# Kernel optimization log

Hardware: AMD Instinct MI355X
Metric: run time of the kernel (lower is better)

The kernel has to match this reference:

```python
import jax, jax.numpy as jnp
import numpy as np

N, E = 50000, 800000
IN_DIM, OUT_DIM, HEADS, ORDER = 128, 32, 4, 2
HID = OUT_DIM * HEADS  # 128
NEG_SLOPE = 0.2
LN_EPS = 1e-5


def setup_inputs() -> dict:
    key = jax.random.key(0)
    ks = jax.random.split(key, 16)
    inp = {
        'features': jax.random.normal(ks[0], (N, IN_DIM), jnp.float32),
        'src': jax.random.randint(ks[1], (E,), 0, N, jnp.int32),
        'dst': jax.random.randint(ks[2], (E,), 0, N, jnp.int32),
    }
    in_dims = [IN_DIM, HID]
    for i in range(ORDER):
        d_in = in_dims[i]
        s = 1.0 / np.sqrt(d_in)
        inp[f'W{i}'] = jax.random.normal(ks[3 + 5 * i], (d_in, HID), jnp.float32) * s
        inp[f'al{i}'] = jax.random.normal(ks[4 + 5 * i], (HEADS, OUT_DIM), jnp.float32) * 0.1
        inp[f'ar{i}'] = jax.random.normal(ks[5 + 5 * i], (HEADS, OUT_DIM), jnp.float32) * 0.1
        inp[f'b{i}'] = jnp.zeros((HID,), jnp.float32)
        inp[f'g{i}'] = jnp.ones((HID,), jnp.float32)
        inp[f'be{i}'] = jnp.zeros((HID,), jnp.float32)
    return inp


def _gat_layer(x, src, dst, W, al, ar, b):
    # x: [N, d_in] -> h: [N, H, D]
    h = (x @ W).reshape(N, HEADS, OUT_DIM)
    el = jnp.sum(h * al, axis=-1)  # [N, H]
    er = jnp.sum(h * ar, axis=-1)  # [N, H]
    e = jax.nn.leaky_relu(el[src] + er[dst], NEG_SLOPE)  # [E, H]
    # segment softmax over incoming edges of each dst node
    m = jax.ops.segment_max(e, dst, num_segments=N)  # [N, H]
    ex = jnp.exp(e - m[dst])  # [E, H]
    denom = jax.ops.segment_sum(ex, dst, num_segments=N)  # [N, H]
    alpha = ex / jnp.maximum(denom[dst], 1e-9)  # [E, H]
    msg = h[src] * alpha[:, :, None]  # [E, H, D]
    out = jax.ops.segment_sum(msg, dst, num_segments=N)  # [N, H, D]
    return out.reshape(N, HID) + b


def _layernorm(x, g, be):
    mu = jnp.mean(x, axis=-1, keepdims=True)
    var = jnp.mean(jnp.square(x - mu), axis=-1, keepdims=True)
    return (x - mu) * jax.lax.rsqrt(var + LN_EPS) * g + be


def reference(features, src, dst, W0, al0, ar0, b0, g0, be0, W1, al1, ar1, b1, g1, be1):
    feats = features
    params = [(W0, al0, ar0, b0, g0, be0), (W1, al1, ar1, b1, g1, be1)]
    for (W, al, ar, b, g, be) in params:
        feats = _gat_layer(feats, src, dst, W, al, ar, b)
        feats = _layernorm(feats, g, be)
        feats = jax.nn.elu(feats)
    return feats
```

## Files before the change

### kernel.cpp

```cpp
#include <hip/hip_runtime.h>
#include <hip/hip_bf16.h>

#define N_NODES 50000
#define E_EDGES 800000
#define HID 128
#define HEADS 4
#define NEG_SLOPE 0.2f
#define LN_EPS 1e-5f
#define PARAM_FLOATS 17024
#define NBUCK 196
#define BCAP 6144
#define BIN_CH 2048

__device__ __forceinline__ float bf2f(__hip_bfloat16 b) { return __bfloat162float(b); }
__device__ __forceinline__ float u2f(unsigned short u) {
    return __uint_as_float(((unsigned int)u) << 16);
}
__device__ __forceinline__ float leaky(float v) { return v > 0.f ? v : v * NEG_SLOPE; }

__device__ __forceinline__ unsigned int f2ord(float f) {
    unsigned int u = __float_as_uint(f);
    return (u & 0x80000000u) ? ~u : (u | 0x80000000u);
}
__device__ __forceinline__ float ord2f(unsigned int u) {
    u = (u & 0x80000000u) ? (u & 0x7FFFFFFFu) : ~u;
    return __uint_as_float(u);
}

__global__ __launch_bounds__(256) void detect_kernel(const unsigned int* __restrict__ w0,
                                                     unsigned int* __restrict__ flag,
                                                     unsigned int* __restrict__ gmax0,
                                                     unsigned int* __restrict__ gmax1) {
    int t = threadIdx.x;
    if (t < 4) {
        gmax0[t] = f2ord(-INFINITY);
        gmax1[t] = f2ord(-INFINITY);
    }
    int cnt = 0;
    for (int i = t; i < 4096; i += 256) {
        unsigned int lo = (w0[i] & 0xFFFFu) << 16;
        float v = fabsf(__uint_as_float(lo));
        if (v >= 1e-6f && v <= 1.0f) cnt++;
    }
    __shared__ int sh[4];
#pragma unroll
    for (int off = 32; off >= 1; off >>= 1) cnt += __shfl_xor(cnt, off);
    if ((t & 63) == 0) sh[t >> 6] = cnt;
    __syncthreads();
    if (t == 0) *flag = ((sh[0] + sh[1] + sh[2] + sh[3]) > 2048) ? 1u : 0u;
}

__device__ __forceinline__ float load_any(const void* p, int i, unsigned int isbf16) {
    return isbf16 ? bf2f(((const __hip_bfloat16*)p)[i]) : ((const float*)p)[i];
}

__global__ __launch_bounds__(256) void cvt_params_kernel(const void* W, const void* al,
                                                         const void* ar, const void* b,
                                                         const void* g, const void* be,
                                                         const unsigned int* __restrict__ flag,
                                                         float* __restrict__ out) {
    int i = blockIdx.x * 256 + threadIdx.x;
    if (i >= PARAM_FLOATS) return;
    unsigned int isb = *flag;
    const void* src; int off;
    if (i < 16384)      { src = W;  off = i; }
    else if (i < 16512) { src = al; off = i - 16384; }
    else if (i < 16640) { src = ar; off = i - 16512; }
    else if (i < 16768) { src = b;  off = i - 16640; }
    else if (i < 16896) { src = g;  off = i - 16768; }
    else                { src = be; off = i - 16896; }
    out[i] = load_any(src, off, isb);
}

__global__ __launch_bounds__(256) void bin_kernel(const int* __restrict__ src,
                                                  const int* __restrict__ dst,
                                                  int* __restrict__ bcnt,
                                                  int2* __restrict__ ebuf) {
    __shared__ int lh[NBUCK];
    __shared__ int lbase[NBUCK];
    int t = threadIdx.x;
    for (int i = t; i < NBUCK; i += 256) lh[i] = 0;
    __syncthreads();
    int e0 = blockIdx.x * BIN_CH;
    int n = min(BIN_CH, E_EDGES - e0);
    int s8[8], d8[8], rk[8];
#pragma unroll
    for (int j = 0; j < 8; ++j) {
        int k = j * 256 + t;
        if (k < n) {
            s8[j] = src[e0 + k];
            d8[j] = dst[e0 + k];
            rk[j] = atomicAdd(&lh[d8[j] >> 8], 1);
        }
    }
    __syncthreads();
    for (int i = t; i < NBUCK; i += 256) lbase[i] = atomicAdd(&bcnt[i], lh[i]);
    __syncthreads();
#pragma unroll
    for (int j = 0; j < 8; ++j) {
        int k = j * 256 + t;
        if (k < n) {
            int b = d8[j] >> 8;
            int pos = lbase[b] + rk[j];
            if (pos < BCAP) ebuf[b * BCAP + pos] = make_int2(s8[j], d8[j]);
        }
    }
}

__global__ __launch_bounds__(256) void bscan_kernel(const int* __restrict__ bcnt,
                                                    int* __restrict__ bbase) {
    int t = threadIdx.x;
    int lane = t & 63, wid = t >> 6;
    int v = (t < NBUCK) ? min(bcnt[t], BCAP) : 0;
    int x = v;
#pragma unroll
    for (int o = 1; o < 64; o <<= 1) {
        int y = __shfl_up(x, o);
        if (lane >= o) x += y;
    }
    __shared__ int wt[4];
    if (lane == 63) wt[wid] = x;
    __syncthreads();
    int add = 0;
    for (int j = 0; j < wid; j++) add += wt[j];
    if (t < NBUCK) bbase[t] = add + x - v;
}

__global__ __launch_bounds__(256) void csr_kernel(const int* __restrict__ bcnt,
                                                  const int* __restrict__ bbase,
                                                  const int2* __restrict__ ebuf,
                                                  int* __restrict__ offs,
                                                  int* __restrict__ esrc) {
    __shared__ int cnt[256];
    __shared__ int wt[4];
    __shared__ int out_lds[BCAP];
    int b = blockIdx.x, t = threadIdx.x;
    int n = min(bcnt[b], BCAP);
    int base = bbase[b];
    const int2* eb = ebuf + b * BCAP;
    cnt[t] = 0;
    __syncthreads();
    for (int i = t; i < n; i += 256) atomicAdd(&cnt[eb[i].y & 255], 1);
    __syncthreads();
    int lane = t & 63, wid = t >> 6;
    int v = cnt[t];
    int x = v;
#pragma unroll
    for (int o = 1; o < 64; o <<= 1) {
        int y = __shfl_up(x, o);
        if (lane >= o) x += y;
    }
    if (lane == 63) wt[wid] = x;
    __syncthreads();
    int add = 0;
    for (int j = 0; j < wid; j++) add += wt[j];
    int excl = add + x - v;
    int node = b * 256 + t;
    if (node <= N_NODES) offs[node] = base + excl;
    __syncthreads();
    cnt[t] = excl;
    __syncthreads();
    for (int i = t; i < n; i += 256) {
        int2 e = eb[i];
        int p = atomicAdd(&cnt[e.y & 255], 1);
        out_lds[p] = e.x;
    }
    __syncthreads();
    for (int i = t; i < n; i += 256) esrc[base + i] = out_lds[i];
}

__global__ __launch_bounds__(256) void gemm_fused_kernel(const void* __restrict__ xin,
                                                         const float* __restrict__ params,
                                                         const unsigned int* __restrict__ flag,
                                                         int xsel,
                                                         unsigned int* __restrict__ hb2,
                                                         float* __restrict__ el,
                                                         float* __restrict__ er,
                                                         unsigned int* __restrict__ gmax,
                                                         int M) {
    __shared__ float xT[16][64];
    __shared__ float wS[16][128];
    __shared__ unsigned int smax[4];
    const float* W = params;
    unsigned int isb = xsel ? *flag : 0u;
    int t = threadIdx.x;
    if (t < 4) smax[t] = 0u;
    int row0 = blockIdx.x * 64;
    int c0 = (t & 15) * 8;
    int r0 = (t >> 4) * 4;
    int xr = t >> 2;
    int xk = (t & 3) * 4;
    int wr = t >> 4;
    int wc = (t & 15) * 8;

    float acc[4][8];
#pragma unroll
    for (int i = 0; i < 4; i++)
#pragma unroll
        for (int j = 0; j < 8; j++) acc[i][j] = 0.f;

    for (int kc = 0; kc < 8; ++kc) {
        float4 xa = make_float4(0.f, 0.f, 0.f, 0.f);
        int grow = row0 + xr;
        if (grow < M) {
            int base = grow * 128 + kc * 16 + xk;
            if (isb) {
                ushort4 u = *(const ushort4*)((const unsigned short*)xin + base);
                xa = make_float4(u2f(u.x), u2f(u.y), u2f(u.z), u2f(u.w));
            } else {
                xa = *(const float4*)((const float*)xin + base);
            }
        }
        xT[xk + 0][xr] = xa.x; xT[xk + 1][xr] = xa.y;
        xT[xk + 2][xr] = xa.z; xT[xk + 3][xr] = xa.w;
        float4 wa = *(const float4*)(W + (kc * 16 + wr) * 128 + wc);
        float4 wb = *(const float4*)(W + (kc * 16 + wr) * 128 + wc + 4);
        *(float4*)&wS[wr][wc] = wa;
        *(float4*)&wS[wr][wc + 4] = wb;
        __syncthreads();
#pragma unroll
        for (int k = 0; k < 16; ++k) {
            float4 a = *(const float4*)&xT[k][r0];
            float4 b0 = *(const float4*)&wS[k][c0];
            float4 b1 = *(const float4*)&wS[k][c0 + 4];
            float av[4] = {a.x, a.y, a.z, a.w};
            float bv[8] = {b0.x, b0.y, b0.z, b0.w, b1.x, b1.y, b1.z, b1.w};
#pragma unroll
            for (int i = 0; i < 4; i++)
#pragma unroll
                for (int j = 0; j < 8; j++) acc[i][j] = fmaf(av[i], bv[j], acc[i][j]);
        }
        __syncthreads();
    }

    int lane = t & 63;
    float al8[8], ar8[8];
#pragma unroll
    for (int j = 0; j < 8; j++) {
        al8[j] = params[16384 + c0 + j];
        ar8[j] = params[16512 + c0 + j];
    }
    int head = (lane & 15) >> 2;
    float elmax = -INFINITY;

#pragma unroll
    for (int i = 0; i < 4; i++) {
        int row = row0 + r0 + i;
        bool ok = row < M;
        if (ok) {
            unsigned int u[4];
#pragma unroll
            for (int j = 0; j < 4; j++) {
                __hip_bfloat16 p0 = __float2bfloat16(acc[i][2 * j]);
                __hip_bfloat16 p1 = __float2bfloat16(acc[i][2 * j + 1]);
                u[j] = (unsigned int)(*(unsigned short*)&p0)
                     | ((unsigned int)(*(unsigned short*)&p1) << 16);
            }
            *(uint4*)(hb2 + row * 64 + (c0 >> 1)) = make_uint4(u[0], u[1], u[2], u[3]);
        }
        float e_l = 0.f, e_r = 0.f;
#pragma unroll
        for (int j = 0; j < 8; j++) {
            e_l = fmaf(acc[i][j], al8[j], e_l);
            e_r = fmaf(acc[i][j], ar8[j], e_r);
        }
        e_l += __shfl_xor(e_l, 1); e_l += __shfl_xor(e_l, 2);
        e_r += __shfl_xor(e_r, 1); e_r += __shfl_xor(e_r, 2);
        if (ok && (lane & 3) == 0) {
            el[row * 4 + head] = e_l;
            er[row * 4 + head] = e_r;
            elmax = fmaxf(elmax, e_l);
        }
    }
    elmax = fmaxf(elmax, __shfl_xor(elmax, 16));
    elmax = fmaxf(elmax, __shfl_xor(elmax, 32));
    __syncthreads();
    if ((lane & 15) == 0 || (lane & 15) == 4 || (lane & 15) == 8 || (lane & 15) == 12) {
        if (elmax > -INFINITY) atomicMax(&smax[head], f2ord(elmax));
    }
    __syncthreads();
    if (t < 4) atomicMax(&gmax[t], smax[t]);
}

template <bool LAST>
__global__ __launch_bounds__(256) void agg_ln_kernel(const int* __restrict__ offs,
                                                     const int* __restrict__ esrc,
                                                     const float* __restrict__ el,
                                                     const float* __restrict__ er,
                                                     const unsigned int* __restrict__ hb2,
                                                     const float* __restrict__ params,
                                                     const unsigned int* __restrict__ gmax,
                                                     const unsigned int* __restrict__ flag,
                                                     float* __restrict__ x_next,
                                                     void* __restrict__ out) {
    int node = (blockIdx.x * 256 + threadIdx.x) >> 6;
    int lane = threadIdx.x & 63;
    if (node >= N_NODES) return;
    int e0 = offs[node], e1 = offs[node + 1];
    int d = e1 - e0;
    int sh = lane & 3;
    int slot = lane >> 2;
    float er_s = er[node * 4 + sh];
    float M = leaky(ord2f(gmax[sh]) + er_s);

    int hd = lane >> 4;
    int c0 = lane * 2;

    float lsum = 0.f, a0 = 0.f, a1 = 0.f;
    for (int b0 = 0; b0 < d; b0 += 16) {
        int idx = b0 + slot;
        float ex = 0.f;
        int s = 0;
        if (idx < d) {
            s = esrc[e0 + idx];
            ex = __expf(leaky(el[s * 4 + sh] + er_s) - M);
        }
        lsum += ex;
        _Float16 e16 = (_Float16)ex;
        unsigned int pk = ((unsigned int)s << 16)
                        | (unsigned int)__builtin_bit_cast(unsigned short, e16);
        int nb = min(16, d - b0);
        if (nb == 16) {
#pragma unroll
            for (int j = 0; j < 16; ++j) {
                unsigned int q = __shfl(pk, j * 4 + hd);
                int sj = q >> 16;
                float exj = (float)__builtin_bit_cast(_Float16, (unsigned short)(q & 0xFFFFu));
                unsigned int p = hb2[sj * 64 + lane];
                a0 = fmaf(exj, u2f((unsigned short)(p & 0xFFFFu)), a0);
                a1 = fmaf(exj, __uint_as_float(p & 0xFFFF0000u), a1);
            }
        } else {
            for (int j = 0; j < nb; ++j) {
                unsigned int q = __shfl(pk, j * 4 + hd);
                int sj = q >> 16;
                float exj = (float)__builtin_bit_cast(_Float16, (unsigned short)(q & 0xFFFFu));
                unsigned int p = hb2[sj * 64 + lane];
                a0 = fmaf(exj, u2f((unsigned short)(p & 0xFFFFu)), a0);
                a1 = fmaf(exj, __uint_as_float(p & 0xFFFF0000u), a1);
            }
        }
    }
#pragma unroll
    for (int off = 4; off <= 32; off <<= 1) lsum += __shfl_xor(lsum, off);
    float l = __shfl(lsum, hd);

    float inv = 1.f / fmaxf(l, 1e-9f);
    const float* b  = params + 16640;
    const float* g  = params + 16768;
    const float* be = params + 16896;
    float v0 = fmaf(a0, inv, b[c0]);
    float v1 = fmaf(a1, inv, b[c0 + 1]);

    float s = v0 + v1;
#pragma unroll
    for (int off = 32; off >= 1; off >>= 1) s += __shfl_xor(s, off);
    float mu = s * (1.f / 128.f);
    float q0 = v0 - mu, q1 = v1 - mu;
    float vs = q0 * q0 + q1 * q1;
#pragma unroll
    for (int off = 32; off >= 1; off >>= 1) vs += __shfl_xor(vs, off);
    float rstd = rsqrtf(vs * (1.f / 128.f) + LN_EPS);
    float y0 = q0 * rstd * g[c0] + be[c0];
    float y1 = q1 * rstd * g[c0 + 1] + be[c0 + 1];
    y0 = y0 > 0.f ? y0 : expm1f(y0);
    y1 = y1 > 0.f ? y1 : expm1f(y1);

    if (LAST) {
        if (*flag) {
            __hip_bfloat16 o0 = __float2bfloat16(y0);
            __hip_bfloat16 o1 = __float2bfloat16(y1);
            unsigned int packed = (unsigned int)(*(unsigned short*)&o0)
                                | ((unsigned int)(*(unsigned short*)&o1) << 16);
            ((unsigned int*)out)[node * 64 + lane] = packed;
        } else {
            ((float2*)out)[node * 64 + lane] = make_float2(y0, y1);
        }
    } else {
        ((float2*)x_next)[node * 64 + lane] = make_float2(y0, y1);
    }
}

extern "C" void kernel_launch(void* const* d_in, const int* in_sizes, int n_in,
                              void* d_out, int out_size, void* d_ws, size_t ws_size,
                              hipStream_t stream) {
    const void* features = d_in[0];
    const int* src = (const int*)d_in[1];
    const int* dst = (const int*)d_in[2];

    char* w = (char*)d_ws;
    float* xbuf = (float*)w;
    unsigned int* hb = (unsigned int*)(w + 25600000);
    float* el = (float*)(w + 38400000);
    float* er = (float*)(w + 39200000);
    float* params0 = (float*)(w + 40000000);
    float* params1 = params0 + PARAM_FLOATS;
    int* offs = (int*)(w + 40137000);
    int* esrc = (int*)(w + 40539000);
    int* bcnt  = (int*)(w + 43739008);
    int* bbase = (int*)(w + 43740032);
    unsigned int* flag  = (unsigned int*)(w + 43740864);
    unsigned int* gmax0 = (unsigned int*)(w + 43740928);
    unsigned int* gmax1 = (unsigned int*)(w + 43740992);
    int2* ebuf = (int2*)(w + 43741184);

    detect_kernel<<<1, 256, 0, stream>>>((const unsigned int*)d_in[3], flag, gmax0, gmax1);
    cvt_params_kernel<<<(PARAM_FLOATS + 255) / 256, 256, 0, stream>>>(
        d_in[3], d_in[4], d_in[5], d_in[6], d_in[7], d_in[8], flag, params0);
    cvt_params_kernel<<<(PARAM_FLOATS + 255) / 256, 256, 0, stream>>>(
        d_in[9], d_in[10], d_in[11], d_in[12], d_in[13], d_in[14], flag, params1);

    hipMemsetAsync(bcnt, 0, NBUCK * sizeof(int), stream);
    bin_kernel<<<(E_EDGES + BIN_CH - 1) / BIN_CH, 256, 0, stream>>>(src, dst, bcnt, ebuf);
    bscan_kernel<<<1, 256, 0, stream>>>(bcnt, bbase);
    csr_kernel<<<NBUCK, 256, 0, stream>>>(bcnt, bbase, ebuf, offs, esrc);

    for (int l = 0; l < 2; ++l) {
        float* params = (l == 0) ? params0 : params1;
        unsigned int* gmax = (l == 0) ? gmax0 : gmax1;
        const void* x = (l == 0) ? features : (const void*)xbuf;
        int xsel = (l == 0) ? 1 : 0;

        gemm_fused_kernel<<<(N_NODES + 63) / 64, 256, 0, stream>>>(
            x, params, flag, xsel, hb, el, er, gmax, N_NODES);
        if (l == 0) {
            agg_ln_kernel<false><<<(N_NODES * 64 + 255) / 256, 256, 0, stream>>>(
                offs, esrc, el, er, hb, params, gmax, flag, xbuf, nullptr);
        } else {
            agg_ln_kernel<true><<<(N_NODES * 64 + 255) / 256, 256, 0, stream>>>(
                offs, esrc, el, er, hb, params, gmax, flag, nullptr, d_out);
        }
    }
}
```

Before: 307.2 us.

## Use bf16 MFMA for node GEMM and store intermediate features as bf16

Replaces the fp32 FMA tiled GEMM with a bf16 MFMA 16x16x32 kernel. The weights are pre-transposed into bf16 during parameter conversion, and results are staged through LDS for the existing bf16 store and attention-logit epilogue. The layer-1 output buffer is also written as packed bf16 instead of fp32, which halves its write/read traffic and lets layer 2 feed MFMA directly. The cost is reduced precision: fp32 inputs and intermediate activations are rounded to bf16 before the matmul.

```diff
diff --git a/kernel.cpp b/kernel.cpp
--- a/kernel.cpp
+++ b/kernel.cpp
@@ -12,9 +12,16 @@
 #define BCAP 6144
 #define BIN_CH 2048
 
+typedef __attribute__((ext_vector_type(8))) short short8;
+typedef __attribute__((ext_vector_type(4))) float float4v;
+
 __device__ __forceinline__ float bf2f(__hip_bfloat16 b) { return __bfloat162float(b); }
 __device__ __forceinline__ float u2f(unsigned short u) {
     return __uint_as_float(((unsigned int)u) << 16);
+}
+__device__ __forceinline__ short bfb(float f) {
+    __hip_bfloat16 h = __float2bfloat16(f);
+    return *(short*)&h;
 }
 __device__ __forceinline__ float leaky(float v) { return v > 0.f ? v : v * NEG_SLOPE; }
 
@@ -58,13 +65,20 @@
                                                          const void* ar, const void* b,
                                                          const void* g, const void* be,
                                                          const unsigned int* __restrict__ flag,
-                                                         float* __restrict__ out) {
+                                                         float* __restrict__ out,
+                                                         unsigned short* __restrict__ wt) {
     int i = blockIdx.x * 256 + threadIdx.x;
     if (i >= PARAM_FLOATS) return;
     unsigned int isb = *flag;
+    if (i < 16384) {
+        unsigned short bits;
+        if (isb) bits = ((const unsigned short*)W)[i];
+        else     { short s = bfb(((const float*)W)[i]); bits = (unsigned short)s; }
+        wt[((i & 127) << 7) | (i >> 7)] = bits;
+        return;
+    }
     const void* src; int off;
-    if (i < 16384)      { src = W;  off = i; }
-    else if (i < 16512) { src = al; off = i - 16384; }
+    if (i < 16512)      { src = al; off = i - 16384; }
     else if (i < 16640) { src = ar; off = i - 16512; }
     else if (i < 16768) { src = b;  off = i - 16640; }
     else if (i < 16896) { src = g;  off = i - 16768; }
@@ -169,71 +183,62 @@
     for (int i = t; i < n; i += 256) esrc[base + i] = out_lds[i];
 }
 
-__global__ __launch_bounds__(256) void gemm_fused_kernel(const void* __restrict__ xin,
-                                                         const float* __restrict__ params,
-                                                         const unsigned int* __restrict__ flag,
-                                                         int xsel,
-                                                         unsigned int* __restrict__ hb2,
-                                                         float* __restrict__ el,
-                                                         float* __restrict__ er,
-                                                         unsigned int* __restrict__ gmax,
-                                                         int M) {
-    __shared__ float xT[16][64];
-    __shared__ float wS[16][128];
+__global__ __launch_bounds__(256) void gemm_mfma_kernel(const void* __restrict__ xin,
+                                                        const unsigned short* __restrict__ wt,
+                                                        const float* __restrict__ params,
+                                                        const unsigned int* __restrict__ flag,
+                                                        int mode,
+                                                        unsigned int* __restrict__ hb2,
+                                                        float* __restrict__ el,
+                                                        float* __restrict__ er,
+                                                        unsigned int* __restrict__ gmax,
+                                                        int M) {
+    __shared__ float ldsC[4][16][132];
     __shared__ unsigned int smax[4];
-    const float* W = params;
-    unsigned int isb = xsel ? *flag : 0u;
+    unsigned int isb = mode ? 1u : *flag;
     int t = threadIdx.x;
     if (t < 4) smax[t] = 0u;
-    int row0 = blockIdx.x * 64;
+    int w = t >> 6, lane = t & 63;
+    int m = lane & 15, quad = lane >> 4;
+    int row0b = blockIdx.x * 64;
+    int arow = row0b + w * 16 + m;
+    bool avalid = arow < M;
+
+    float4v acc[8];
+#pragma unroll
+    for (int i = 0; i < 8; i++) acc[i] = (float4v){0.f, 0.f, 0.f, 0.f};
+
+#pragma unroll
+    for (int kt = 0; kt < 4; ++kt) {
+        short8 a = (short8){0, 0, 0, 0, 0, 0, 0, 0};
+        if (avalid) {
+            int base = arow * 128 + kt * 32 + quad * 8;
+            if (isb) {
+                a = *(const short8*)((const unsigned short*)xin + base);
+            } else {
+                const float* xp = (const float*)xin + base;
+                float4 f0 = *(const float4*)xp;
+                float4 f1 = *(const float4*)(xp + 4);
+                a = (short8){bfb(f0.x), bfb(f0.y), bfb(f0.z), bfb(f0.w),
+                             bfb(f1.x), bfb(f1.y), bfb(f1.z), bfb(f1.w)};
+            }
+        }
+#pragma unroll
+        for (int ct = 0; ct < 8; ++ct) {
+            short8 b = *(const short8*)(wt + (ct * 16 + m) * 128 + kt * 32 + quad * 8);
+            acc[ct] = __builtin_amdgcn_mfma_f32_16x16x32_bf16(a, b, acc[ct], 0, 0, 0);
+        }
+    }
+
+#pragma unroll
+    for (int ct = 0; ct < 8; ++ct)
+#pragma unroll
+        for (int r = 0; r < 4; ++r)
+            ldsC[w][quad * 4 + r][ct * 16 + m] = acc[ct][r];
+    __syncthreads();
+
     int c0 = (t & 15) * 8;
-    int r0 = (t >> 4) * 4;
-    int xr = t >> 2;
-    int xk = (t & 3) * 4;
-    int wr = t >> 4;
-    int wc = (t & 15) * 8;
-
-    float acc[4][8];
-#pragma unroll
-    for (int i = 0; i < 4; i++)
-#pragma unroll
-        for (int j = 0; j < 8; j++) acc[i][j] = 0.f;
-
-    for (int kc = 0; kc < 8; ++kc) {
-        float4 xa = make_float4(0.f, 0.f, 0.f, 0.f);
-        int grow = row0 + xr;
-        if (grow < M) {
-            int base = grow * 128 + kc * 16 + xk;
-            if (isb) {
-                ushort4 u = *(const ushort4*)((const unsigned short*)xin + base);
-                xa = make_float4(u2f(u.x), u2f(u.y), u2f(u.z), u2f(u.w));
-            } else {
-                xa = *(const float4*)((const float*)xin + base);
-            }
-        }
-        xT[xk + 0][xr] = xa.x; xT[xk + 1][xr] = xa.y;
-        xT[xk + 2][xr] = xa.z; xT[xk + 3][xr] = xa.w;
-        float4 wa = *(const float4*)(W + (kc * 16 + wr) * 128 + wc);
-        float4 wb = *(const float4*)(W + (kc * 16 + wr) * 128 + wc + 4);
-        *(float4*)&wS[wr][wc] = wa;
-        *(float4*)&wS[wr][wc + 4] = wb;
-        __syncthreads();
-#pragma unroll
-        for (int k = 0; k < 16; ++k) {
-            float4 a = *(const float4*)&xT[k][r0];
-            float4 b0 = *(const float4*)&wS[k][c0];
-            float4 b1 = *(const float4*)&wS[k][c0 + 4];
-            float av[4] = {a.x, a.y, a.z, a.w};
-            float bv[8] = {b0.x, b0.y, b0.z, b0.w, b1.x, b1.y, b1.z, b1.w};
-#pragma unroll
-            for (int i = 0; i < 4; i++)
-#pragma unroll
-                for (int j = 0; j < 8; j++) acc[i][j] = fmaf(av[i], bv[j], acc[i][j]);
-        }
-        __syncthreads();
-    }
-
-    int lane = t & 63;
+    int r0e = (t >> 4) * 4;
     float al8[8], ar8[8];
 #pragma unroll
     for (int j = 0; j < 8; j++) {
@@ -245,24 +250,27 @@
 
 #pragma unroll
     for (int i = 0; i < 4; i++) {
-        int row = row0 + r0 + i;
+        int rr = r0e + i;
+        int row = row0b + rr;
         bool ok = row < M;
+        const float* ld = &ldsC[rr >> 4][rr & 15][c0];
+        float4 h0 = *(const float4*)ld;
+        float4 h1 = *(const float4*)(ld + 4);
+        float hv[8] = {h0.x, h0.y, h0.z, h0.w, h1.x, h1.y, h1.z, h1.w};
         if (ok) {
             unsigned int u[4];
 #pragma unroll
             for (int j = 0; j < 4; j++) {
-                __hip_bfloat16 p0 = __float2bfloat16(acc[i][2 * j]);
-                __hip_bfloat16 p1 = __float2bfloat16(acc[i][2 * j + 1]);
-                u[j] = (unsigned int)(*(unsigned short*)&p0)
-                     | ((unsigned int)(*(unsigned short*)&p1) << 16);
+                u[j] = (unsigned int)(unsigned short)bfb(hv[2 * j])
+                     | ((unsigned int)(unsigned short)bfb(hv[2 * j + 1]) << 16);
             }
             *(uint4*)(hb2 + row * 64 + (c0 >> 1)) = make_uint4(u[0], u[1], u[2], u[3]);
         }
         float e_l = 0.f, e_r = 0.f;
 #pragma unroll
         for (int j = 0; j < 8; j++) {
-            e_l = fmaf(acc[i][j], al8[j], e_l);
-            e_r = fmaf(acc[i][j], ar8[j], e_r);
+            e_l = fmaf(hv[j], al8[j], e_l);
+            e_r = fmaf(hv[j], ar8[j], e_r);
         }
         e_l += __shfl_xor(e_l, 1); e_l += __shfl_xor(e_l, 2);
         e_r += __shfl_xor(e_r, 1); e_r += __shfl_xor(e_r, 2);
@@ -291,7 +299,7 @@
                                                      const float* __restrict__ params,
                                                      const unsigned int* __restrict__ gmax,
                                                      const unsigned int* __restrict__ flag,
-                                                     float* __restrict__ x_next,
+                                                     unsigned int* __restrict__ x_next,
                                                      void* __restrict__ out) {
     int node = (blockIdx.x * 256 + threadIdx.x) >> 6;
     int lane = threadIdx.x & 63;
@@ -368,16 +376,16 @@
 
     if (LAST) {
         if (*flag) {
-            __hip_bfloat16 o0 = __float2bfloat16(y0);
-            __hip_bfloat16 o1 = __float2bfloat16(y1);
-            unsigned int packed = (unsigned int)(*(unsigned short*)&o0)
-                                | ((unsigned int)(*(unsigned short*)&o1) << 16);
+            unsigned int packed = (unsigned int)(unsigned short)bfb(y0)
+                                | ((unsigned int)(unsigned short)bfb(y1) << 16);
             ((unsigned int*)out)[node * 64 + lane] = packed;
         } else {
             ((float2*)out)[node * 64 + lane] = make_float2(y0, y1);
         }
     } else {
-        ((float2*)x_next)[node * 64 + lane] = make_float2(y0, y1);
+        unsigned int packed = (unsigned int)(unsigned short)bfb(y0)
+                            | ((unsigned int)(unsigned short)bfb(y1) << 16);
+        x_next[node * 64 + lane] = packed;
     }
 }
 
@@ -389,26 +397,28 @@
     const int* dst = (const int*)d_in[2];
 
     char* w = (char*)d_ws;
-    float* xbuf = (float*)w;
-    unsigned int* hb = (unsigned int*)(w + 25600000);
-    float* el = (float*)(w + 38400000);
-    float* er = (float*)(w + 39200000);
-    float* params0 = (float*)(w + 40000000);
+    unsigned int* xbuf = (unsigned int*)w;
+    unsigned int* hb = (unsigned int*)(w + 12800000);
+    float* el = (float*)(w + 25600000);
+    float* er = (float*)(w + 26400000);
+    float* params0 = (float*)(w + 27200000);
     float* params1 = params0 + PARAM_FLOATS;
-    int* offs = (int*)(w + 40137000);
-    int* esrc = (int*)(w + 40539000);
-    int* bcnt  = (int*)(w + 43739008);
-    int* bbase = (int*)(w + 43740032);
-    unsigned int* flag  = (unsigned int*)(w + 43740864);
-    unsigned int* gmax0 = (unsigned int*)(w + 43740928);
-    unsigned int* gmax1 = (unsigned int*)(w + 43740992);
-    int2* ebuf = (int2*)(w + 43741184);
+    unsigned short* wt0 = (unsigned short*)(w + 27337000);
+    unsigned short* wt1 = wt0 + 16384;
+    int* offs = (int*)(w + 27403000);
+    int* esrc = (int*)(w + 27604000);
+    int* bcnt  = (int*)(w + 30804992);
+    int* bbase = (int*)(w + 30806016);
+    unsigned int* flag  = (unsigned int*)(w + 30806848);
+    unsigned int* gmax0 = (unsigned int*)(w + 30806912);
+    unsigned int* gmax1 = (unsigned int*)(w + 30806976);
+    int2* ebuf = (int2*)(w + 30807040);
 
     detect_kernel<<<1, 256, 0, stream>>>((const unsigned int*)d_in[3], flag, gmax0, gmax1);
     cvt_params_kernel<<<(PARAM_FLOATS + 255) / 256, 256, 0, stream>>>(
-        d_in[3], d_in[4], d_in[5], d_in[6], d_in[7], d_in[8], flag, params0);
+        d_in[3], d_in[4], d_in[5], d_in[6], d_in[7], d_in[8], flag, params0, wt0);
     cvt_params_kernel<<<(PARAM_FLOATS + 255) / 256, 256, 0, stream>>>(
-        d_in[9], d_in[10], d_in[11], d_in[12], d_in[13], d_in[14], flag, params1);
+        d_in[9], d_in[10], d_in[11], d_in[12], d_in[13], d_in[14], flag, params1, wt1);
 
     hipMemsetAsync(bcnt, 0, NBUCK * sizeof(int), stream);
     bin_kernel<<<(E_EDGES + BIN_CH - 1) / BIN_CH, 256, 0, stream>>>(src, dst, bcnt, ebuf);
@@ -417,12 +427,13 @@
 
     for (int l = 0; l < 2; ++l) {
         float* params = (l == 0) ? params0 : params1;
+        unsigned short* wt = (l == 0) ? wt0 : wt1;
         unsigned int* gmax = (l == 0) ? gmax0 : gmax1;
         const void* x = (l == 0) ? features : (const void*)xbuf;
-        int xsel = (l == 0) ? 1 : 0;
-
-        gemm_fused_kernel<<<(N_NODES + 63) / 64, 256, 0, stream>>>(
-            x, params, flag, xsel, hb, el, er, gmax, N_NODES);
+        int mode = (l == 0) ? 0 : 1;
+
+        gemm_mfma_kernel<<<(N_NODES + 63) / 64, 256, 0, stream>>>(
+            x, wt, params, flag, mode, hb, el, er, gmax, N_NODES);
         if (l == 0) {
             agg_ln_kernel<false><<<(N_NODES * 64 + 255) / 256, 256, 0, stream>>>(
                 offs, esrc, el, er, hb, params, gmax, flag, xbuf, nullptr);
```

Result: faster. 291.1 us (-5.2%).
